# Optimization experiments

Hardware: AMD Instinct MI355X
Metric: run time of the kernel (lower is better)

## Reference

```python
import jax, jax.numpy as jnp
import numpy as np

# config constants (assumed; see notes)
OSC_COUPLING = 0.1
AMP_DECAY = 0.1
AMP_SAT = 1.0
HOPF_MU = 1.0
H = 1024
N_OSC = 64  # min(N_OSCILLATORS=64, H//8=128)


def leaky_relu(x, slope=0.2):
    return jnp.where(x >= 0, x, slope * x)


def setup_inputs() -> dict:
    key = jax.random.key(0)
    ks = jax.random.split(key, 16)
    B, S = 4, 2048
    sc_h = 1.0 / np.sqrt(H)
    sc_2n = 1.0 / np.sqrt(2 * N_OSC)
    return {
        "x": jax.random.normal(ks[0], (B, S, H), jnp.float32),
        "t": jax.random.uniform(ks[1], (B, S, 1), jnp.float32),
        # to_oscillator: Linear(H,H) -> LeakyReLU -> Linear(H, 2*N_OSC)
        "W1": jax.random.normal(ks[2], (H, H), jnp.float32) * sc_h,
        "b1": jnp.zeros((H,), jnp.float32),
        "W2": jax.random.normal(ks[3], (H, 2 * N_OSC), jnp.float32) * sc_h,
        "b2": jnp.zeros((2 * N_OSC,), jnp.float32),
        # from_oscillator: Linear(2*N_OSC,H) -> LeakyReLU -> Linear(H,H)
        "W3": jax.random.normal(ks[4], (2 * N_OSC, H), jnp.float32) * sc_2n,
        "b3": jnp.zeros((H,), jnp.float32),
        "W4": jax.random.normal(ks[5], (H, H), jnp.float32) * sc_h,
        "b4": jnp.zeros((H,), jnp.float32),
        # time_mod: Linear(1, N_OSC)
        "Wt": jax.random.normal(ks[6], (1, N_OSC), jnp.float32),
        "bt": jnp.zeros((N_OSC,), jnp.float32),
        "coupling": jax.random.normal(ks[7], (N_OSC, N_OSC), jnp.float32) * OSC_COUPLING,
        "frequencies": jnp.linspace(0.5, 2.0, N_OSC, dtype=jnp.float32),
        "mu": jnp.float32(HOPF_MU),
    }


def reference(x, t, W1, b1, W2, b2, W3, b3, W4, b4, Wt, bt, coupling, frequencies, mu):
    n = frequencies.shape[0]
    # to_oscillator MLP
    h = leaky_relu(x @ W1 + b1)
    osc = h @ W2 + b2                       # [B,S,2n]
    phase, amplitude = osc[..., :n], osc[..., n:]
    t_mod = t @ Wt + bt                      # [B,S,n]

    # NOTE: original loop reads phase[:, i-1] / amplitude[:, i-1] from the
    # ORIGINAL tensors, so steps are independent -> vectorize over time.
    pp = phase[:, :-1]                       # [B,S-1,n] prev phase
    diff = pp[..., :, None] - pp[..., None, :]   # [B,S-1,n,n]
    # sum over last dim of sin(diff) @ coupling == einsum with coupling row-sums
    csum = coupling.sum(axis=1)              # [n]
    coupling_sum = jnp.einsum('bsjm,m->bsj', jnp.sin(diff), csum)
    dphase = frequencies + coupling_sum * OSC_COUPLING + t_mod[:, 1:] * 0.1
    phase_new = pp + dphase * 0.1

    ap = amplitude[:, :-1]
    damp = (-AMP_DECAY + mu) * ap - ap ** 3
    amp_new = jnp.tanh(ap + damp * 0.1) * AMP_SAT

    phase_out = jnp.concatenate([phase[:, :1], phase_new], axis=1)
    amp_out = jnp.concatenate([amplitude[:, :1], amp_new], axis=1)
    combined = jnp.concatenate([phase_out, amp_out], axis=-1)  # [B,S,2n]

    # from_oscillator MLP
    h2 = leaky_relu(combined @ W3 + b3)
    oscillator_output = h2 @ W4 + b4
    return x + oscillator_output * 0.1
```

## Files before the change

kernel.cpp:

```cpp
#include <hip/hip_runtime.h>
#include <hip/hip_bf16.h>

typedef __hip_bfloat16 bf16;
typedef __attribute__((ext_vector_type(4))) float f32x4;
typedef __attribute__((ext_vector_type(8))) short short8;

#define BM 128
#define BN 128
#define BK 64
#define MROWS 8192
#define PARTSZ (MROWS * 128)

__device__ __forceinline__ void gload_lds16(const void* g, void* l) {
  __builtin_amdgcn_global_load_lds((const __attribute__((address_space(1))) void*)g,
                                   (__attribute__((address_space(3))) void*)l, 16, 0, 0);
}

template<int EPI, bool SWZ>
__global__ __launch_bounds__(256)
void gemm_kernel(const bf16* __restrict__ A, const bf16* __restrict__ Bt,
                 const float* __restrict__ bias, const float* __restrict__ X,
                 void* __restrict__ Cout, int M, int N, int K, int kLen)
{
  __shared__ bf16 As[2][BM * BK];
  __shared__ bf16 Bs[2][BN * BK];
  const int tid  = threadIdx.x;
  const int lane = tid & 63;
  const int wr   = (tid >> 6) >> 1;
  const int wc   = (tid >> 6) & 1;

  int bmI, bnI;
  if (SWZ) {
    const int nwg = gridDim.x * gridDim.y;
    const int bid = blockIdx.x + gridDim.x * blockIdx.y;
    const int cpx = nwg >> 3;
    const int swz = (bid & 7) * cpx + (bid >> 3);
    bmI = swz % gridDim.x;
    bnI = swz / gridDim.x;
  } else {
    bmI = blockIdx.x;
    bnI = blockIdx.y;
  }
  const long bm = (long)bmI * BM;
  const long bn = (long)bnI * BN;
  const int kOff = blockIdx.z * kLen;

  f32x4 acc[4][4] = {};

  int frow[4], fcol[4], fdst[4];
#pragma unroll
  for (int c = 0; c < 4; ++c) {
    int f    = (c * 256 + tid) * 16;
    int row  = f >> 7;
    int bcol = (f & 127) ^ ((row & 7) << 4);
    frow[c] = row;
    fcol[c] = bcol >> 1;
    fdst[c] = f;
  }

  const bf16* Abase = A  + bm * (long)K + kOff;
  const bf16* Bbase = Bt + bn * (long)K + kOff;

#define STAGE(kt, buf)                                                          \
  do {                                                                          \
    const long kb_ = (long)(kt) * BK;                                           \
    _Pragma("unroll")                                                           \
    for (int c = 0; c < 4; ++c) {                                               \
      gload_lds16(Abase + (long)frow[c] * K + kb_ + fcol[c],                    \
                  (char*)As[buf] + fdst[c]);                                    \
      gload_lds16(Bbase + (long)frow[c] * K + kb_ + fcol[c],                    \
                  (char*)Bs[buf] + fdst[c]);                                    \
    }                                                                           \
  } while (0)

  const int nK = kLen / BK;
  STAGE(0, 0);
  for (int kt = 0; kt < nK; ++kt) {
    const int cur = kt & 1;
    if (kt + 1 < nK) {
      STAGE(kt + 1, cur ^ 1);
      asm volatile("s_waitcnt vmcnt(8)" ::: "memory");
    } else {
      asm volatile("s_waitcnt vmcnt(0)" ::: "memory");
    }
    __builtin_amdgcn_s_barrier();
    __builtin_amdgcn_sched_barrier(0);

#pragma unroll
    for (int ks = 0; ks < 2; ++ks) {
      short8 af[4], bfr[4];
      const int kcolb = (ks * 32 + (lane >> 4) * 8) * 2;
#pragma unroll
      for (int m = 0; m < 4; ++m) {
        int rr = wr * 64 + m * 16 + (lane & 15);
        af[m] = *(const short8*)((const char*)As[cur] + rr * 128 + (kcolb ^ ((rr & 7) << 4)));
      }
#pragma unroll
      for (int n = 0; n < 4; ++n) {
        int rr = wc * 64 + n * 16 + (lane & 15);
        bfr[n] = *(const short8*)((const char*)Bs[cur] + rr * 128 + (kcolb ^ ((rr & 7) << 4)));
      }
#pragma unroll
      for (int m = 0; m < 4; ++m)
#pragma unroll
        for (int n = 0; n < 4; ++n)
          acc[m][n] = __builtin_amdgcn_mfma_f32_16x16x32_bf16(af[m], bfr[n], acc[m][n], 0, 0, 0);
    }
    __builtin_amdgcn_s_barrier();
  }
#undef STAGE

  char* Cbase = (char*)Cout;
  if (EPI == 1) Cbase += (size_t)blockIdx.z * M * (size_t)N * 4;
#pragma unroll
  for (int n = 0; n < 4; ++n) {
    const long col = bn + wc * 64 + n * 16 + (lane & 15);
    const float bv = (EPI == 1) ? 0.f : bias[col];
#pragma unroll
    for (int m = 0; m < 4; ++m) {
      const long row0 = bm + wr * 64 + m * 16 + ((lane >> 4) << 2);
#pragma unroll
      for (int q = 0; q < 4; ++q) {
        float v = acc[m][n][q] + bv;
        const long idx = (row0 + q) * (long)N + col;
        if (EPI == 0) {
          v = (v >= 0.f) ? v : 0.2f * v;
          ((bf16*)Cbase)[idx] = __float2bfloat16(v);
        } else if (EPI == 1) {
          ((float*)Cbase)[idx] = v;
        } else {
          ((float*)Cbase)[idx] = X[idx] + 0.1f * v;
        }
      }
    }
  }
}

__device__ __forceinline__ void transpose_tile(const float* __restrict__ in,
                                               bf16* __restrict__ out,
                                               int R, int C, int bx, int by, int tid)
{
  __shared__ float tile[32][33];
  const int tx = tid & 31, ty = tid >> 5;
#pragma unroll
  for (int i = ty; i < 32; i += 8)
    tile[i][tx] = in[(size_t)(by * 32 + i) * C + bx * 32 + tx];
  __syncthreads();
#pragma unroll
  for (int i = ty; i < 32; i += 8)
    out[(size_t)(bx * 32 + i) * R + by * 32 + tx] = __float2bfloat16(tile[tx][i]);
}

__global__ void prep_kernel(const float* __restrict__ x, bf16* __restrict__ xb,
                            const float* __restrict__ W1, bf16* __restrict__ W1t,
                            const float* __restrict__ W2, bf16* __restrict__ W2t,
                            const float* __restrict__ W3, bf16* __restrict__ W3t,
                            const float* __restrict__ W4, bf16* __restrict__ W4t,
                            const float* __restrict__ coupling, float* __restrict__ csum)
{
  const int b = blockIdx.x;
  const int tid = threadIdx.x;
  if (b < 2048) {
    const int n4 = MROWS * 1024 / 4;
    for (int i = b * 256 + tid; i < n4; i += 2048 * 256) {
      const float4 v = ((const float4*)x)[i];
      union { bf16 h[4]; uint2 u; } pk;
      pk.h[0] = __float2bfloat16(v.x); pk.h[1] = __float2bfloat16(v.y);
      pk.h[2] = __float2bfloat16(v.z); pk.h[3] = __float2bfloat16(v.w);
      ((uint2*)xb)[i] = pk.u;
    }
  } else if (b < 3072) {
    const int tb = b - 2048;
    transpose_tile(W1, W1t, 1024, 1024, tb & 31, tb >> 5, tid);
  } else if (b < 4096) {
    const int tb = b - 3072;
    transpose_tile(W4, W4t, 1024, 1024, tb & 31, tb >> 5, tid);
  } else if (b < 4224) {
    const int tb = b - 4096;
    transpose_tile(W2, W2t, 1024, 128, tb & 3, tb >> 2, tid);
  } else if (b < 4352) {
    const int tb = b - 4224;
    transpose_tile(W3, W3t, 128, 1024, tb & 31, tb >> 5, tid);
  } else {
    if (tid < 64) {
      float s = 0.f;
#pragma unroll
      for (int n = 0; n < 64; ++n) s += coupling[tid * 64 + n];
      csum[tid] = s;
    }
  }
}

__global__ void middle_kernel(const float* __restrict__ osc_part, const float* __restrict__ t,
                              const float* __restrict__ Wt, const float* __restrict__ bt,
                              const float* __restrict__ freq, const float* __restrict__ csum,
                              const float* __restrict__ mu_p, const float* __restrict__ b2,
                              bf16* __restrict__ combined, int nrows, int S)
{
  const int r = blockIdx.x * 4 + (threadIdx.x >> 6);
  const int j = threadIdx.x & 63;
  if (r >= nrows) return;
  const int s = r & (S - 1);
  const int src = (s == 0) ? r : r - 1;
  const size_t rs = (size_t)src * 128;

  float p = b2[j], a = b2[64 + j];
#pragma unroll
  for (int kc = 0; kc < 4; ++kc) {
    p += osc_part[(size_t)kc * PARTSZ + rs + j];
    a += osc_part[(size_t)kc * PARTSZ + rs + 64 + j];
  }

  float ph, am;
  if (s == 0) {
    ph = p; am = a;
  } else {
    float sp, cp;
    sincosf(p, &sp, &cp);
    const float cw = csum[j];
    float sumc = cp * cw, sums = sp * cw;
#pragma unroll
    for (int off = 32; off; off >>= 1) {
      sumc += __shfl_xor(sumc, off);
      sums += __shfl_xor(sums, off);
    }
    const float coupling_sum = sp * sumc - cp * sums;
    const float tm = t[r] * Wt[j] + bt[j];
    const float dp = freq[j] + coupling_sum * 0.1f + tm * 0.1f;
    ph = p + dp * 0.1f;
    const float mu = mu_p[0];
    const float u = a + 0.1f * ((mu - 0.1f) * a - a * a * a);
    am = tanhf(u);
  }
  combined[(size_t)r * 128 + j]      = __float2bfloat16(ph);
  combined[(size_t)r * 128 + 64 + j] = __float2bfloat16(am);
}

extern "C" void kernel_launch(void* const* d_in, const int* in_sizes, int n_in,
                              void* d_out, int out_size, void* d_ws, size_t ws_size,
                              hipStream_t stream)
{
  const float* x        = (const float*)d_in[0];
  const float* t        = (const float*)d_in[1];
  const float* W1       = (const float*)d_in[2];
  const float* b1       = (const float*)d_in[3];
  const float* W2       = (const float*)d_in[4];
  const float* b2       = (const float*)d_in[5];
  const float* W3       = (const float*)d_in[6];
  const float* b3       = (const float*)d_in[7];
  const float* W4       = (const float*)d_in[8];
  const float* b4       = (const float*)d_in[9];
  const float* Wt       = (const float*)d_in[10];
  const float* bt       = (const float*)d_in[11];
  const float* coupling = (const float*)d_in[12];
  const float* freq     = (const float*)d_in[13];
  const float* mu       = (const float*)d_in[14];

  const int Mrows = MROWS;
  const int S     = 2048;

  char* ws = (char*)d_ws;
  size_t o = 0;
  auto alloc = [&](size_t bytes) {
    char* p = ws + o;
    o = (o + bytes + 255) & ~(size_t)255;
    return p;
  };
  bf16* xw_h2    = (bf16*)alloc((size_t)Mrows * 1024 * 2);
  bf16* hbuf     = (bf16*)alloc((size_t)Mrows * 1024 * 2);
  bf16* W1t      = (bf16*)alloc((size_t)1024 * 1024 * 2);
  bf16* W4t      = (bf16*)alloc((size_t)1024 * 1024 * 2);
  bf16* W2t      = (bf16*)alloc((size_t)1024 * 128 * 2);
  bf16* W3t      = (bf16*)alloc((size_t)1024 * 128 * 2);
  float* oscp    = (float*)alloc((size_t)4 * PARTSZ * 4);
  bf16* combined = (bf16*)alloc((size_t)Mrows * 128 * 2);
  float* csum    = (float*)alloc(64 * 4);

  prep_kernel<<<4353, 256, 0, stream>>>(x, xw_h2, W1, W1t, W2, W2t, W3, W3t, W4, W4t,
                                        coupling, csum);

  gemm_kernel<0, true><<<dim3(64, 8), 256, 0, stream>>>(xw_h2, W1t, b1, nullptr, hbuf,
                                                        Mrows, 1024, 1024, 1024);
  gemm_kernel<1, false><<<dim3(64, 1, 4), 256, 0, stream>>>(hbuf, W2t, nullptr, nullptr, oscp,
                                                            Mrows, 128, 1024, 256);
  middle_kernel<<<Mrows / 4, 256, 0, stream>>>(oscp, t, Wt, bt, freq, csum, mu, b2,
                                               combined, Mrows, S);
  gemm_kernel<0, true><<<dim3(64, 8), 256, 0, stream>>>(combined, W3t, b3, nullptr, xw_h2,
                                                        Mrows, 1024, 128, 128);
  gemm_kernel<2, true><<<dim3(64, 8), 256, 0, stream>>>(xw_h2, W4t, b4, x, d_out,
                                                        Mrows, 1024, 1024, 1024);
}
```

Measured before the change: 192.0 us.

## Enlarge GEMM tile to 256x128 with 8 waves and triple-buffered LDS pipeline

Doubles the M tile to 256 rows, runs 512 threads per block, and replaces the double-buffered LDS staging with a three-slot ring so two k-tiles are in flight ahead of compute. The aim is more operand reuse per block and better hiding of global-to-LDS latency. In exchange it halves the grid and uses about 144 KB of LDS, limiting occupancy to one block per CU, and the short-K GEMMs gain little from deeper prefetch.

```diff
diff --git a/kernel.cpp b/kernel.cpp
--- a/kernel.cpp
+++ b/kernel.cpp
@@ -5,29 +5,32 @@
 typedef __attribute__((ext_vector_type(4))) float f32x4;
 typedef __attribute__((ext_vector_type(8))) short short8;
 
-#define BM 128
+#define BM 256
 #define BN 128
 #define BK 64
 #define MROWS 8192
 #define PARTSZ (MROWS * 128)
 
+#define A_BYTES 32768
+#define SLOT_BYTES 49152
+
 __device__ __forceinline__ void gload_lds16(const void* g, void* l) {
   __builtin_amdgcn_global_load_lds((const __attribute__((address_space(1))) void*)g,
                                    (__attribute__((address_space(3))) void*)l, 16, 0, 0);
 }
 
 template<int EPI, bool SWZ>
-__global__ __launch_bounds__(256)
+__global__ __launch_bounds__(512)
 void gemm_kernel(const bf16* __restrict__ A, const bf16* __restrict__ Bt,
                  const float* __restrict__ bias, const float* __restrict__ X,
                  void* __restrict__ Cout, int M, int N, int K, int kLen)
 {
-  __shared__ bf16 As[2][BM * BK];
-  __shared__ bf16 Bs[2][BN * BK];
+  __shared__ char smem[3 * SLOT_BYTES];
   const int tid  = threadIdx.x;
   const int lane = tid & 63;
-  const int wr   = (tid >> 6) >> 1;
-  const int wc   = (tid >> 6) & 1;
+  const int wid  = tid >> 6;
+  const int wr   = wid >> 1;
+  const int wc   = wid & 1;
 
   int bmI, bnI;
   if (SWZ) {
@@ -47,45 +50,57 @@
 
   f32x4 acc[4][4] = {};
 
-  int frow[4], fcol[4], fdst[4];
+  int frowA[4], fcolA[4], fdstA[4];
 #pragma unroll
   for (int c = 0; c < 4; ++c) {
-    int f    = (c * 256 + tid) * 16;
+    int f    = (c * 512 + tid) * 16;
     int row  = f >> 7;
     int bcol = (f & 127) ^ ((row & 7) << 4);
-    frow[c] = row;
-    fcol[c] = bcol >> 1;
-    fdst[c] = f;
+    frowA[c] = row; fcolA[c] = bcol >> 1; fdstA[c] = f;
+  }
+  int frowB[2], fcolB[2], fdstB[2];
+#pragma unroll
+  for (int c = 0; c < 2; ++c) {
+    int f    = (c * 512 + tid) * 16;
+    int row  = f >> 7;
+    int bcol = (f & 127) ^ ((row & 7) << 4);
+    frowB[c] = row; fcolB[c] = bcol >> 1; fdstB[c] = f;
   }
 
   const bf16* Abase = A  + bm * (long)K + kOff;
   const bf16* Bbase = Bt + bn * (long)K + kOff;
 
-#define STAGE(kt, buf)                                                          \
+#define STAGE(kt, slot)                                                         \
   do {                                                                          \
     const long kb_ = (long)(kt) * BK;                                           \
+    char* sb_ = smem + (slot) * SLOT_BYTES;                                     \
     _Pragma("unroll")                                                           \
-    for (int c = 0; c < 4; ++c) {                                               \
-      gload_lds16(Abase + (long)frow[c] * K + kb_ + fcol[c],                    \
-                  (char*)As[buf] + fdst[c]);                                    \
-      gload_lds16(Bbase + (long)frow[c] * K + kb_ + fcol[c],                    \
-                  (char*)Bs[buf] + fdst[c]);                                    \
-    }                                                                           \
+    for (int c = 0; c < 4; ++c)                                                 \
+      gload_lds16(Abase + (long)frowA[c] * K + kb_ + fcolA[c], sb_ + fdstA[c]); \
+    _Pragma("unroll")                                                           \
+    for (int c = 0; c < 2; ++c)                                                 \
+      gload_lds16(Bbase + (long)frowB[c] * K + kb_ + fcolB[c],                  \
+                  sb_ + A_BYTES + fdstB[c]);                                    \
   } while (0)
 
   const int nK = kLen / BK;
   STAGE(0, 0);
+  STAGE(1, 1);
+  int slot = 0;
   for (int kt = 0; kt < nK; ++kt) {
-    const int cur = kt & 1;
-    if (kt + 1 < nK) {
-      STAGE(kt + 1, cur ^ 1);
-      asm volatile("s_waitcnt vmcnt(8)" ::: "memory");
+    if (kt + 2 < nK) {
+      STAGE(kt + 2, (slot + 2) % 3);
+      asm volatile("s_waitcnt vmcnt(12)" ::: "memory");
+    } else if (kt + 1 < nK) {
+      asm volatile("s_waitcnt vmcnt(6)" ::: "memory");
     } else {
       asm volatile("s_waitcnt vmcnt(0)" ::: "memory");
     }
     __builtin_amdgcn_s_barrier();
     __builtin_amdgcn_sched_barrier(0);
 
+    const char* As = smem + slot * SLOT_BYTES;
+    const char* Bs = As + A_BYTES;
 #pragma unroll
     for (int ks = 0; ks < 2; ++ks) {
       short8 af[4], bfr[4];
@@ -93,12 +108,12 @@
 #pragma unroll
       for (int m = 0; m < 4; ++m) {
         int rr = wr * 64 + m * 16 + (lane & 15);
-        af[m] = *(const short8*)((const char*)As[cur] + rr * 128 + (kcolb ^ ((rr & 7) << 4)));
+        af[m] = *(const short8*)(As + rr * 128 + (kcolb ^ ((rr & 7) << 4)));
       }
 #pragma unroll
       for (int n = 0; n < 4; ++n) {
         int rr = wc * 64 + n * 16 + (lane & 15);
-        bfr[n] = *(const short8*)((const char*)Bs[cur] + rr * 128 + (kcolb ^ ((rr & 7) << 4)));
+        bfr[n] = *(const short8*)(Bs + rr * 128 + (kcolb ^ ((rr & 7) << 4)));
       }
 #pragma unroll
       for (int m = 0; m < 4; ++m)
@@ -107,6 +122,7 @@
           acc[m][n] = __builtin_amdgcn_mfma_f32_16x16x32_bf16(af[m], bfr[n], acc[m][n], 0, 0, 0);
     }
     __builtin_amdgcn_s_barrier();
+    slot = (slot + 1) % 3;
   }
 #undef STAGE
 
@@ -279,14 +295,14 @@
   prep_kernel<<<4353, 256, 0, stream>>>(x, xw_h2, W1, W1t, W2, W2t, W3, W3t, W4, W4t,
                                         coupling, csum);
 
-  gemm_kernel<0, true><<<dim3(64, 8), 256, 0, stream>>>(xw_h2, W1t, b1, nullptr, hbuf,
+  gemm_kernel<0, true><<<dim3(32, 8), 512, 0, stream>>>(xw_h2, W1t, b1, nullptr, hbuf,
                                                         Mrows, 1024, 1024, 1024);
-  gemm_kernel<1, false><<<dim3(64, 1, 4), 256, 0, stream>>>(hbuf, W2t, nullptr, nullptr, oscp,
+  gemm_kernel<1, false><<<dim3(32, 1, 4), 512, 0, stream>>>(hbuf, W2t, nullptr, nullptr, oscp,
                                                             Mrows, 128, 1024, 256);
   middle_kernel<<<Mrows / 4, 256, 0, stream>>>(oscp, t, Wt, bt, freq, csum, mu, b2,
                                                combined, Mrows, S);
-  gemm_kernel<0, true><<<dim3(64, 8), 256, 0, stream>>>(combined, W3t, b3, nullptr, xw_h2,
+  gemm_kernel<0, true><<<dim3(32, 8), 512, 0, stream>>>(combined, W3t, b3, nullptr, xw_h2,
                                                         Mrows, 1024, 128, 128);
-  gemm_kernel<2, true><<<dim3(64, 8), 256, 0, stream>>>(xw_h2, W4t, b4, x, d_out,
+  gemm_kernel<2, true><<<dim3(32, 8), 512, 0, stream>>>(xw_h2, W4t, b4, x, d_out,
                                                         Mrows, 1024, 1024, 1024);
 }
```

New measurement: 194.7 us. Within noise of the previous version (+1.4%).
